# Kernel optimization log

Measured on AMD Instinct MI355X. Metric: run time of the kernel, lower is better.

## Reference

```python
import jax, jax.numpy as jnp
import numpy as np

EPS = 1e-8  # torch cosine_similarity eps


def _first_occurrence_mask(ids, n, k, half):
    # ids: [half] int indices into [0,n). Returns boolean mask of the first k
    # distinct ids in order of first occurrence (torch.unique + slice semantics).
    pos = jnp.arange(half, dtype=jnp.int32)
    occ = jnp.full((n,), half, dtype=jnp.int32).at[ids].min(pos)  # first occurrence position, half if absent
    order = jnp.argsort(occ)
    rank = jnp.zeros((n,), jnp.int32).at[order].set(jnp.arange(n, dtype=jnp.int32))
    return (rank < k) & (occ < half)


def _split_rows(emb, mask, k):
    # emb: [n,h]; selected rows (mask) go to 'mutual' (in index order, zero-padded
    # to k), remaining rows go to 'only' (in index order, zero-padded).
    n = emb.shape[0]
    idx = jnp.arange(n)
    order = jnp.argsort(jnp.where(mask, idx, idx + n))  # selected first, index order
    sel_first = mask[order]
    g = emb[order]
    mutual = g[:k] * sel_first[:k, None].astype(emb.dtype)
    only = g[k:] * (~sel_first[k:])[:, None].astype(emb.dtype)
    return mutual, only


def _split_one(v, t, kv, kt, half):
    # v: [Vl,H], t: [Tl,H]
    Vl, H = v.shape
    Tl = t.shape[0]
    vnorm = jnp.linalg.norm(v, axis=-1)  # [Vl]
    tnorm = jnp.linalg.norm(t, axis=-1)  # [Tl]
    sims = (v @ t.T) / jnp.maximum(vnorm[:, None] * tnorm[None, :], EPS)  # [Vl,Tl]
    top_idx = jnp.argsort(-sims.reshape(-1))[:half]
    vid = (top_idx // Tl).astype(jnp.int32)
    tid = (top_idx % Tl).astype(jnp.int32)
    mask_v = _first_occurrence_mask(vid, Vl, kv, half)
    mask_t = _first_occurrence_mask(tid, Tl, kt, half)
    v_mut, v_only = _split_rows(v, mask_v, kv)
    t_mut, t_only = _split_rows(t, mask_t, kt)
    return v_mut, t_mut, v_only, t_only


def setup_inputs() -> dict:
    key = jax.random.key(0)
    k1, k2 = jax.random.split(key)
    B, Vl, Tl, H = 64, 256, 512, 512
    return {
        "video_embeddings": jax.random.normal(k1, (B, Vl, H), dtype=jnp.float32),
        "text_embeddings": jax.random.normal(k2, (B, Tl, H), dtype=jnp.float32),
    }


def reference(video_embeddings, text_embeddings):
    B, Vl, H = video_embeddings.shape
    Tl = text_embeddings.shape[1]
    half = (Vl * Tl) // 2
    kv = (Vl - 1) // 2  # replicates source loop-variable slice bug
    kt = (Tl - 1) // 2
    fn = lambda v, t: _split_one(v, t, kv, kt, half)
    return jax.vmap(fn)(video_embeddings, text_embeddings)
```

## Files before the change

kernel.cpp:

```cpp
#include <hip/hip_runtime.h>
#include <math.h>

#define B_  64
#define VL 256
#define TL 512
#define HD 512
#define KV 127
#define KT 255
#define EPSF 1e-8f

typedef __attribute__((ext_vector_type(8))) short short8;
typedef __attribute__((ext_vector_type(4))) float f32x4;

#define WS_ROWP  0
#define WS_COLP  (B_*2*VL)
#define WS_SRC   (WS_COLP + B_*2*TL)

__device__ __forceinline__ unsigned fkey(float f) {
    unsigned u = __float_as_uint(f);
    return (u & 0x80000000u) ? ~u : (u | 0x80000000u);
}

__device__ __forceinline__ unsigned cvt_pk_bf16(float a, float b) {
    unsigned r;
    asm("v_cvt_pk_bf16_f32 %0, %1, %2" : "=v"(r) : "v"(a), "v"(b));
    return r;
}

__device__ __forceinline__ void split_pair(float a, float b, unsigned& hh, unsigned& ll, float& ss) {
    ss = fmaf(a, a, ss);
    ss = fmaf(b, b, ss);
    unsigned ua = __float_as_uint(a) & 0xFFFF0000u;
    unsigned ub = __float_as_uint(b) & 0xFFFF0000u;
    hh = __builtin_amdgcn_perm(ub, ua, 0x07060302u);
    ll = cvt_pk_bf16(a - __uint_as_float(ua), b - __uint_as_float(ub));
}

__device__ __forceinline__ void cvt_store8(unsigned* __restrict__ ph, unsigned* __restrict__ pl,
                                           float4 x0, float4 x1, float& ss) {
    unsigned hh0, hh1, hh2, hh3, ll0, ll1, ll2, ll3;
    split_pair(x0.x, x0.y, hh0, ll0, ss);
    split_pair(x0.z, x0.w, hh1, ll1, ss);
    split_pair(x1.x, x1.y, hh2, ll2, ss);
    split_pair(x1.z, x1.w, hh3, ll3, ss);
    *(uint4*)ph = (uint4){hh0, hh1, hh2, hh3};
    *(uint4*)pl = (uint4){ll0, ll1, ll2, ll3};
}

__global__ __launch_bounds__(512, 2) void k_simmax(const float* __restrict__ video,
                                                   const float* __restrict__ text,
                                                   unsigned* __restrict__ rowp,
                                                   unsigned* __restrict__ colp) {
    __shared__ __align__(16) unsigned pA[2][2][2048];
    __shared__ __align__(16) unsigned pB[2][2][4096];
    __shared__ float vns_s[128], tns_s[256];
    __shared__ unsigned rowm[128], colm[256];

    int bb = blockIdx.x;
    int z = bb & 7, w = bb >> 3;
    int b  = z * 8 + (w >> 2);
    int mt = (w >> 1) & 1, nt = w & 1;
    int m0 = mt * 128, n0 = nt * 256;

    const float* Vb = video + (size_t)b * VL * HD;
    const float* Tb = text  + (size_t)b * TL * HD;

    int tid = threadIdx.x;
    int l = tid & 63, wid = tid >> 6;
    int fr = l & 15, g = l >> 4;
    int wm = (wid >> 2) * 64, wn = (wid & 3) * 64;

    int rA = tid >> 2, c = tid & 3;
    int rB0 = rA, rB1 = 128 + rA;
    unsigned wA  = rA  * 16 + (c ^ ((rA  >> 1) & 3)) * 4;
    unsigned wB0 = rB0 * 16 + (c ^ ((rB0 >> 1) & 3)) * 4;
    unsigned wB1 = rB1 * 16 + (c ^ ((rB1 >> 1) & 3)) * 4;
    const float* aptr  = Vb + (size_t)(m0 + rA)  * HD + c * 8;
    const float* bptr0 = Tb + (size_t)(n0 + rB0) * HD + c * 8;
    const float* bptr1 = Tb + (size_t)(n0 + rB1) * HD + c * 8;

    f32x4 acc[4][4];
#pragma unroll
    for (int i = 0; i < 4; ++i)
#pragma unroll
        for (int j = 0; j < 4; ++j) acc[i][j] = (f32x4){0.f, 0.f, 0.f, 0.f};

    float sa = 0.f, sb0 = 0.f, sb1 = 0.f;

    float4 a0  = *(const float4*)(aptr),      a1  = *(const float4*)(aptr + 4);
    float4 b00 = *(const float4*)(bptr0),     b01 = *(const float4*)(bptr0 + 4);
    float4 b10 = *(const float4*)(bptr1),     b11 = *(const float4*)(bptr1 + 4);
    cvt_store8(&pA[0][0][wA],  &pA[0][1][wA],  a0,  a1,  sa);
    cvt_store8(&pB[0][0][wB0], &pB[0][1][wB0], b00, b01, sb0);
    cvt_store8(&pB[0][0][wB1], &pB[0][1][wB1], b10, b11, sb1);
    a0  = *(const float4*)(aptr + 32);  a1  = *(const float4*)(aptr + 36);
    b00 = *(const float4*)(bptr0 + 32); b01 = *(const float4*)(bptr0 + 36);
    b10 = *(const float4*)(bptr1 + 32); b11 = *(const float4*)(bptr1 + 36);
    __syncthreads();

    for (int t = 0; t < 16; ++t) {
        int cur = t & 1, nxt = cur ^ 1;
        short8 fah[4], fal[4], fbh[4], fbl[4];
#pragma unroll
        for (int i = 0; i < 4; ++i) {
            int row = wm + i * 16 + fr;
            unsigned ridx = row * 16 + (g ^ ((row >> 1) & 3)) * 4;
            fah[i] = *(const short8*)&pA[cur][0][ridx];
            fal[i] = *(const short8*)&pA[cur][1][ridx];
        }
#pragma unroll
        for (int j = 0; j < 4; ++j) {
            int row = wn + j * 16 + fr;
            unsigned ridx = row * 16 + (g ^ ((row >> 1) & 3)) * 4;
            fbh[j] = *(const short8*)&pB[cur][0][ridx];
            fbl[j] = *(const short8*)&pB[cur][1][ridx];
        }
        if (t < 15) {
            cvt_store8(&pA[nxt][0][wA],  &pA[nxt][1][wA],  a0,  a1,  sa);
            cvt_store8(&pB[nxt][0][wB0], &pB[nxt][1][wB0], b00, b01, sb0);
            cvt_store8(&pB[nxt][0][wB1], &pB[nxt][1][wB1], b10, b11, sb1);
            if (t < 14) {
                const float* ap  = aptr  + (t + 2) * 32;
                const float* bp0 = bptr0 + (t + 2) * 32;
                const float* bp1 = bptr1 + (t + 2) * 32;
                a0  = *(const float4*)ap;  a1  = *(const float4*)(ap + 4);
                b00 = *(const float4*)bp0; b01 = *(const float4*)(bp0 + 4);
                b10 = *(const float4*)bp1; b11 = *(const float4*)(bp1 + 4);
            }
        }
#pragma unroll
        for (int j = 0; j < 4; ++j)
#pragma unroll
            for (int i = 0; i < 4; ++i)
                acc[i][j] = __builtin_amdgcn_mfma_f32_16x16x32_bf16(fah[i], fbh[j], acc[i][j], 0, 0, 0);
#pragma unroll
        for (int j = 0; j < 4; ++j)
#pragma unroll
            for (int i = 0; i < 4; ++i)
                acc[i][j] = __builtin_amdgcn_mfma_f32_16x16x32_bf16(fal[i], fbh[j], acc[i][j], 0, 0, 0);
#pragma unroll
        for (int j = 0; j < 4; ++j)
#pragma unroll
            for (int i = 0; i < 4; ++i)
                acc[i][j] = __builtin_amdgcn_mfma_f32_16x16x32_bf16(fah[i], fbl[j], acc[i][j], 0, 0, 0);
        __syncthreads();
    }

    sa  += __shfl_xor(sa, 1, 64);  sa  += __shfl_xor(sa, 2, 64);
    sb0 += __shfl_xor(sb0, 1, 64); sb0 += __shfl_xor(sb0, 2, 64);
    sb1 += __shfl_xor(sb1, 1, 64); sb1 += __shfl_xor(sb1, 2, 64);
    if (c == 0) {
        vns_s[rA]  = sqrtf(sa);
        tns_s[rB0] = sqrtf(sb0);
        tns_s[rB1] = sqrtf(sb1);
    }
    if (tid < 128) rowm[tid] = 0u;
    if (tid >= 128 && tid < 384) colm[tid - 128] = 0u;
    __syncthreads();

    float vr[16], tc[4];
#pragma unroll
    for (int i = 0; i < 4; ++i)
#pragma unroll
        for (int r = 0; r < 4; ++r) vr[i * 4 + r] = vns_s[wm + i * 16 + g * 4 + r];
#pragma unroll
    for (int j = 0; j < 4; ++j) tc[j] = tns_s[wn + j * 16 + fr];

    float rmx[16], cmx[4];
#pragma unroll
    for (int i = 0; i < 16; ++i) rmx[i] = -INFINITY;
#pragma unroll
    for (int j = 0; j < 4; ++j) cmx[j] = -INFINITY;
#pragma unroll
    for (int i = 0; i < 4; ++i)
#pragma unroll
        for (int j = 0; j < 4; ++j)
#pragma unroll
            for (int r = 0; r < 4; ++r) {
                float s = acc[i][j][r] / fmaxf(vr[i * 4 + r] * tc[j], EPSF);
                rmx[i * 4 + r] = fmaxf(rmx[i * 4 + r], s);
                cmx[j]         = fmaxf(cmx[j], s);
            }
#pragma unroll
    for (int off = 1; off < 16; off <<= 1)
#pragma unroll
        for (int i = 0; i < 16; ++i) rmx[i] = fmaxf(rmx[i], __shfl_xor(rmx[i], off, 64));
#pragma unroll
    for (int off = 16; off < 64; off <<= 1)
#pragma unroll
        for (int j = 0; j < 4; ++j) cmx[j] = fmaxf(cmx[j], __shfl_xor(cmx[j], off, 64));
    if (fr == 0) {
#pragma unroll
        for (int i = 0; i < 4; ++i)
#pragma unroll
            for (int r = 0; r < 4; ++r)
                atomicMax(&rowm[wm + i * 16 + g * 4 + r], fkey(rmx[i * 4 + r]));
    }
    if (g == 0) {
#pragma unroll
        for (int j = 0; j < 4; ++j) atomicMax(&colm[wn + j * 16 + fr], fkey(cmx[j]));
    }
    __syncthreads();
    if (tid < 128)      rowp[(b * 2 + nt) * VL + m0 + tid] = rowm[tid];
    else if (tid < 384) colp[(b * 2 + mt) * TL + n0 + (tid - 128)] = colm[tid - 128];
}

__global__ __launch_bounds__(512) void k_select(const unsigned* __restrict__ rowp,
                                                const unsigned* __restrict__ colp,
                                                int* __restrict__ srcidx) {
    __shared__ __align__(16) unsigned rk[VL];
    __shared__ __align__(16) unsigned ck[TL];
    __shared__ int wsumv[4], wsumt[8];
    int b = blockIdx.x, tid = threadIdx.x;
    int lane = tid & 63, wv = tid >> 6;
    if (tid < VL) rk[tid] = max(rowp[(b * 2 + 0) * VL + tid], rowp[(b * 2 + 1) * VL + tid]);
    ck[tid] = max(colp[(b * 2 + 0) * TL + tid], colp[(b * 2 + 1) * TL + tid]);
    for (int i = tid; i < 768; i += 512) srcidx[b * 768 + i] = -1;
    __syncthreads();

    int flagv = 0;
    if (tid < VL) {
        unsigned me = rk[tid];
        int cnt = 0;
        for (int jb = 0; jb < VL / 4; ++jb) {
            uint4 k4 = *(const uint4*)&rk[jb * 4];
            cnt += (k4.x > me) + (k4.y > me) + (k4.z > me) + (k4.w > me);
            cnt += (k4.x == me && (jb * 4 + 0) < tid) + (k4.y == me && (jb * 4 + 1) < tid)
                 + (k4.z == me && (jb * 4 + 2) < tid) + (k4.w == me && (jb * 4 + 3) < tid);
        }
        flagv = (cnt < KV) ? 1 : 0;
    }
    int flagt;
    {
        unsigned me = ck[tid];
        int cnt = 0;
        for (int jb = 0; jb < TL / 4; ++jb) {
            uint4 k4 = *(const uint4*)&ck[jb * 4];
            cnt += (k4.x > me) + (k4.y > me) + (k4.z > me) + (k4.w > me);
            cnt += (k4.x == me && (jb * 4 + 0) < tid) + (k4.y == me && (jb * 4 + 1) < tid)
                 + (k4.z == me && (jb * 4 + 2) < tid) + (k4.w == me && (jb * 4 + 3) < tid);
        }
        flagt = (cnt < KT) ? 1 : 0;
    }

    unsigned long long mv = __ballot(flagv);
    unsigned long long mtk = __ballot(flagt);
    if (lane == 0) {
        if (wv < 4) wsumv[wv] = __popcll(mv);
        wsumt[wv] = __popcll(mtk);
    }
    __syncthreads();

    unsigned long long ltmask = (1ull << lane) - 1ull;
    if (tid < VL) {
        int base = 0;
#pragma unroll
        for (int w2 = 0; w2 < 4; ++w2) base += (w2 < wv) ? wsumv[w2] : 0;
        int mV = wsumv[0] + wsumv[1] + wsumv[2] + wsumv[3];
        int ps = base + __popcll(mv & ltmask);
        int pu = tid - ps;
        if (flagv) srcidx[b * 768 + ps] = tid;
        else {
            int pos = pu - (KV - mV);
            if (pos >= 0 && pos < VL - KV) srcidx[b * 768 + 382 + pos] = tid;
        }
    }
    {
        int base = 0;
#pragma unroll
        for (int w2 = 0; w2 < 8; ++w2) base += (w2 < wv) ? wsumt[w2] : 0;
        int mT = 0;
#pragma unroll
        for (int w2 = 0; w2 < 8; ++w2) mT += wsumt[w2];
        int ps = base + __popcll(mtk & ltmask);
        int pu = tid - ps;
        if (flagt) srcidx[b * 768 + 127 + ps] = tid;
        else {
            int pos = pu - (KT - mT);
            if (pos >= 0 && pos < TL - KT) srcidx[b * 768 + 511 + pos] = tid;
        }
    }
}

__global__ __launch_bounds__(256) void k_gather(const float* __restrict__ video,
                                                const float* __restrict__ text,
                                                const int* __restrict__ srcidx,
                                                float* __restrict__ out) {
    int row  = blockIdx.x * 4 + (threadIdx.x >> 6);
    int lane = threadIdx.x & 63;
    int b, base, L;
    const float* tens;
    const int S0 = B_ * KV, S1 = S0 + B_ * KT, S2 = S1 + B_ * (VL - KV);
    if (row < S0)      { b = row / KV;            base = 0   + row % KV;            tens = video; L = VL; }
    else if (row < S1) { int r = row - S0; b = r / KT;       base = 127 + r % KT;       tens = text;  L = TL; }
    else if (row < S2) { int r = row - S1; b = r / (VL - KV); base = 382 + r % (VL - KV); tens = video; L = VL; }
    else               { int r = row - S2; b = r / (TL - KT); base = 511 + r % (TL - KT); tens = text;  L = TL; }
    int s = srcidx[b * 768 + base];
    float* op = out + (size_t)row * HD;
    if (s >= 0) {
        const float* sp = tens + ((size_t)b * L + s) * HD;
#pragma unroll
        for (int it = 0; it < 2; ++it)
            *(float4*)(op + lane * 4 + it * 256) = *(const float4*)(sp + lane * 4 + it * 256);
    } else {
        float4 zv = {0.f, 0.f, 0.f, 0.f};
#pragma unroll
        for (int it = 0; it < 2; ++it)
            *(float4*)(op + lane * 4 + it * 256) = zv;
    }
}

extern "C" void kernel_launch(void* const* d_in, const int* in_sizes, int n_in,
                              void* d_out, int out_size, void* d_ws, size_t ws_size,
                              hipStream_t stream) {
    const float* video = (const float*)d_in[0];
    const float* text  = (const float*)d_in[1];
    float*    ws     = (float*)d_ws;
    unsigned* rowp   = (unsigned*)(ws + WS_ROWP);
    unsigned* colp   = (unsigned*)(ws + WS_COLP);
    int*      srcidx = (int*)(ws + WS_SRC);
    float*    out    = (float*)d_out;

    k_simmax<<<256,             512, 0, stream>>>(video, text, rowp, colp);
    k_select<<<B_,              512, 0, stream>>>(rowp, colp, srcidx);
    k_gather<<<(B_ * 768) / 4,  256, 0, stream>>>(video, text, srcidx, out);
}
```

Before: 86.65 us.

## Split similarity-max GEMM into 128x128 tiles across 512 blocks; nontemporal gather stores

The similarity/max kernel now uses 128x128 output tiles with 256-thread blocks, so it launches 512 blocks instead of 256 with 512 threads. The aim is to fill more CUs on the 256-CU device and cut the tail imbalance. Row partial maxima grow from 2 to 4 per batch, so the select kernel now reduces four partials. The gather kernel switches to nontemporal stores for its output. The trade-off is that text and video rows are loaded and converted more often across blocks, and rowp needs more workspace.

Result: slower. 89.89 us (+3.7%).

```diff
diff --git a/kernel.cpp b/kernel.cpp
--- a/kernel.cpp
+++ b/kernel.cpp
@@ -13,7 +13,7 @@
 typedef __attribute__((ext_vector_type(4))) float f32x4;
 
 #define WS_ROWP  0
-#define WS_COLP  (B_*2*VL)
+#define WS_COLP  (B_*4*VL)
 #define WS_SRC   (WS_COLP + B_*2*TL)
 
 __device__ __forceinline__ unsigned fkey(float f) {
@@ -47,20 +47,20 @@
     *(uint4*)pl = (uint4){ll0, ll1, ll2, ll3};
 }
 
-__global__ __launch_bounds__(512, 2) void k_simmax(const float* __restrict__ video,
+__global__ __launch_bounds__(256, 2) void k_simmax(const float* __restrict__ video,
                                                    const float* __restrict__ text,
                                                    unsigned* __restrict__ rowp,
                                                    unsigned* __restrict__ colp) {
     __shared__ __align__(16) unsigned pA[2][2][2048];
-    __shared__ __align__(16) unsigned pB[2][2][4096];
-    __shared__ float vns_s[128], tns_s[256];
-    __shared__ unsigned rowm[128], colm[256];
+    __shared__ __align__(16) unsigned pB[2][2][2048];
+    __shared__ float vns_s[128], tns_s[128];
+    __shared__ unsigned rowm[128], colm[128];
 
     int bb = blockIdx.x;
-    int z = bb & 7, w = bb >> 3;
-    int b  = z * 8 + (w >> 2);
-    int mt = (w >> 1) & 1, nt = w & 1;
-    int m0 = mt * 128, n0 = nt * 256;
+    int z = bb & 7, y = (bb >> 3) & 7, x = bb >> 6;
+    int b  = z * 8 + x;
+    int mt = y >> 2, nt = y & 3;
+    int m0 = mt * 128, n0 = nt * 128;
 
     const float* Vb = video + (size_t)b * VL * HD;
     const float* Tb = text  + (size_t)b * TL * HD;
@@ -68,16 +68,15 @@
     int tid = threadIdx.x;
     int l = tid & 63, wid = tid >> 6;
     int fr = l & 15, g = l >> 4;
-    int wm = (wid >> 2) * 64, wn = (wid & 3) * 64;
-
-    int rA = tid >> 2, c = tid & 3;
-    int rB0 = rA, rB1 = 128 + rA;
-    unsigned wA  = rA  * 16 + (c ^ ((rA  >> 1) & 3)) * 4;
-    unsigned wB0 = rB0 * 16 + (c ^ ((rB0 >> 1) & 3)) * 4;
-    unsigned wB1 = rB1 * 16 + (c ^ ((rB1 >> 1) & 3)) * 4;
-    const float* aptr  = Vb + (size_t)(m0 + rA)  * HD + c * 8;
-    const float* bptr0 = Tb + (size_t)(n0 + rB0) * HD + c * 8;
-    const float* bptr1 = Tb + (size_t)(n0 + rB1) * HD + c * 8;
+    int wm = (wid >> 1) * 64, wn = (wid & 1) * 64;
+
+    int rS = tid >> 1;
+    int c0 = (tid & 1) * 2;
+    unsigned sw = (rS >> 1) & 3;
+    unsigned w0 = rS * 16 + ((unsigned)c0       ^ sw) * 4;
+    unsigned w1 = rS * 16 + ((unsigned)(c0 + 1) ^ sw) * 4;
+    const float* aptr = Vb + (size_t)(m0 + rS) * HD + c0 * 8;
+    const float* bptr = Tb + (size_t)(n0 + rS) * HD + c0 * 8;
 
     f32x4 acc[4][4];
 #pragma unroll
@@ -85,17 +84,20 @@
 #pragma unroll
         for (int j = 0; j < 4; ++j) acc[i][j] = (f32x4){0.f, 0.f, 0.f, 0.f};
 
-    float sa = 0.f, sb0 = 0.f, sb1 = 0.f;
-
-    float4 a0  = *(const float4*)(aptr),      a1  = *(const float4*)(aptr + 4);
-    float4 b00 = *(const float4*)(bptr0),     b01 = *(const float4*)(bptr0 + 4);
-    float4 b10 = *(const float4*)(bptr1),     b11 = *(const float4*)(bptr1 + 4);
-    cvt_store8(&pA[0][0][wA],  &pA[0][1][wA],  a0,  a1,  sa);
-    cvt_store8(&pB[0][0][wB0], &pB[0][1][wB0], b00, b01, sb0);
-    cvt_store8(&pB[0][0][wB1], &pB[0][1][wB1], b10, b11, sb1);
-    a0  = *(const float4*)(aptr + 32);  a1  = *(const float4*)(aptr + 36);
-    b00 = *(const float4*)(bptr0 + 32); b01 = *(const float4*)(bptr0 + 36);
-    b10 = *(const float4*)(bptr1 + 32); b11 = *(const float4*)(bptr1 + 36);
+    float sa = 0.f, sb = 0.f;
+
+    float4 a0 = *(const float4*)(aptr),      a1 = *(const float4*)(aptr + 4);
+    float4 a2 = *(const float4*)(aptr + 8),  a3 = *(const float4*)(aptr + 12);
+    float4 b0 = *(const float4*)(bptr),      b1 = *(const float4*)(bptr + 4);
+    float4 b2 = *(const float4*)(bptr + 8),  b3 = *(const float4*)(bptr + 12);
+    cvt_store8(&pA[0][0][w0], &pA[0][1][w0], a0, a1, sa);
+    cvt_store8(&pA[0][0][w1], &pA[0][1][w1], a2, a3, sa);
+    cvt_store8(&pB[0][0][w0], &pB[0][1][w0], b0, b1, sb);
+    cvt_store8(&pB[0][0][w1], &pB[0][1][w1], b2, b3, sb);
+    a0 = *(const float4*)(aptr + 32); a1 = *(const float4*)(aptr + 36);
+    a2 = *(const float4*)(aptr + 40); a3 = *(const float4*)(aptr + 44);
+    b0 = *(const float4*)(bptr + 32); b1 = *(const float4*)(bptr + 36);
+    b2 = *(const float4*)(bptr + 40); b3 = *(const float4*)(bptr + 44);
     __syncthreads();
 
     for (int t = 0; t < 16; ++t) {
@@ -116,16 +118,17 @@
             fbl[j] = *(const short8*)&pB[cur][1][ridx];
         }
         if (t < 15) {
-            cvt_store8(&pA[nxt][0][wA],  &pA[nxt][1][wA],  a0,  a1,  sa);
-            cvt_store8(&pB[nxt][0][wB0], &pB[nxt][1][wB0], b00, b01, sb0);
-            cvt_store8(&pB[nxt][0][wB1], &pB[nxt][1][wB1], b10, b11, sb1);
+            cvt_store8(&pA[nxt][0][w0], &pA[nxt][1][w0], a0, a1, sa);
+            cvt_store8(&pA[nxt][0][w1], &pA[nxt][1][w1], a2, a3, sa);
+            cvt_store8(&pB[nxt][0][w0], &pB[nxt][1][w0], b0, b1, sb);
+            cvt_store8(&pB[nxt][0][w1], &pB[nxt][1][w1], b2, b3, sb);
             if (t < 14) {
-                const float* ap  = aptr  + (t + 2) * 32;
-                const float* bp0 = bptr0 + (t + 2) * 32;
-                const float* bp1 = bptr1 + (t + 2) * 32;
-                a0  = *(const float4*)ap;  a1  = *(const float4*)(ap + 4);
-                b00 = *(const float4*)bp0; b01 = *(const float4*)(bp0 + 4);
-                b10 = *(const float4*)bp1; b11 = *(const float4*)(bp1 + 4);
+                const float* ap = aptr + (t + 2) * 32;
+                const float* bp = bptr + (t + 2) * 32;
+                a0 = *(const float4*)ap;        a1 = *(const float4*)(ap + 4);
+                a2 = *(const float4*)(ap + 8);  a3 = *(const float4*)(ap + 12);
+                b0 = *(const float4*)bp;        b1 = *(const float4*)(bp + 4);
+                b2 = *(const float4*)(bp + 8);  b3 = *(const float4*)(bp + 12);
             }
         }
 #pragma unroll
@@ -146,16 +149,11 @@
         __syncthreads();
     }
 
-    sa  += __shfl_xor(sa, 1, 64);  sa  += __shfl_xor(sa, 2, 64);
-    sb0 += __shfl_xor(sb0, 1, 64); sb0 += __shfl_xor(sb0, 2, 64);
-    sb1 += __shfl_xor(sb1, 1, 64); sb1 += __shfl_xor(sb1, 2, 64);
-    if (c == 0) {
-        vns_s[rA]  = sqrtf(sa);
-        tns_s[rB0] = sqrtf(sb0);
-        tns_s[rB1] = sqrtf(sb1);
-    }
+    sa += __shfl_xor(sa, 1, 64);
+    sb += __shfl_xor(sb, 1, 64);
+    if ((tid & 1) == 0) { vns_s[rS] = sqrtf(sa); tns_s[rS] = sqrtf(sb); }
     if (tid < 128) rowm[tid] = 0u;
-    if (tid >= 128 && tid < 384) colm[tid - 128] = 0u;
+    else           colm[tid - 128] = 0u;
     __syncthreads();
 
     float vr[16], tc[4];
@@ -201,8 +199,8 @@
         for (int j = 0; j < 4; ++j) atomicMax(&colm[wn + j * 16 + fr], fkey(cmx[j]));
     }
     __syncthreads();
-    if (tid < 128)      rowp[(b * 2 + nt) * VL + m0 + tid] = rowm[tid];
-    else if (tid < 384) colp[(b * 2 + mt) * TL + n0 + (tid - 128)] = colm[tid - 128];
+    if (tid < 128) rowp[(b * 4 + nt) * VL + m0 + tid] = rowm[tid];
+    else           colp[(b * 2 + mt) * TL + n0 + (tid - 128)] = colm[tid - 128];
 }
 
 __global__ __launch_bounds__(512) void k_select(const unsigned* __restrict__ rowp,
@@ -213,7 +211,11 @@
     __shared__ int wsumv[4], wsumt[8];
     int b = blockIdx.x, tid = threadIdx.x;
     int lane = tid & 63, wv = tid >> 6;
-    if (tid < VL) rk[tid] = max(rowp[(b * 2 + 0) * VL + tid], rowp[(b * 2 + 1) * VL + tid]);
+    if (tid < VL) {
+        unsigned m = max(max(rowp[(b * 4 + 0) * VL + tid], rowp[(b * 4 + 1) * VL + tid]),
+                         max(rowp[(b * 4 + 2) * VL + tid], rowp[(b * 4 + 3) * VL + tid]));
+        rk[tid] = m;
+    }
     ck[tid] = max(colp[(b * 2 + 0) * TL + tid], colp[(b * 2 + 1) * TL + tid]);
     for (int i = tid; i < 768; i += 512) srcidx[b * 768 + i] = -1;
     __syncthreads();
@@ -300,13 +302,15 @@
     if (s >= 0) {
         const float* sp = tens + ((size_t)b * L + s) * HD;
 #pragma unroll
+        for (int it = 0; it < 2; ++it) {
+            f32x4 v = *(const f32x4*)(sp + lane * 4 + it * 256);
+            __builtin_nontemporal_store(v, (f32x4*)(op + lane * 4 + it * 256));
+        }
+    } else {
+        f32x4 zv = {0.f, 0.f, 0.f, 0.f};
+#pragma unroll
         for (int it = 0; it < 2; ++it)
-            *(float4*)(op + lane * 4 + it * 256) = *(const float4*)(sp + lane * 4 + it * 256);
-    } else {
-        float4 zv = {0.f, 0.f, 0.f, 0.f};
-#pragma unroll
-        for (int it = 0; it < 2; ++it)
-            *(float4*)(op + lane * 4 + it * 256) = zv;
+            __builtin_nontemporal_store(zv, (f32x4*)(op + lane * 4 + it * 256));
     }
 }
 
@@ -321,7 +325,7 @@
     int*      srcidx = (int*)(ws + WS_SRC);
     float*    out    = (float*)d_out;
 
-    k_simmax<<<256,             512, 0, stream>>>(video, text, rowp, colp);
+    k_simmax<<<B_ * 8,          256, 0, stream>>>(video, text, rowp, colp);
     k_select<<<B_,              512, 0, stream>>>(rowp, colp, srcidx);
     k_gather<<<(B_ * 768) / 4,  256, 0, stream>>>(video, text, srcidx, out);
 }
```

## Fuse simmax, select and gather into one kernel with per-batch atomic handoff

Applied to the files above, without the earlier changes.

Merges the three kernels into a single launch. The last of the four tiles of each batch to finish, detected with an atomic counter, runs the top-k selection. The other three tiles spin on a per-batch flag, and then all four tiles gather their share of output rows. This removes two kernel launches and their gaps, at the cost of a memset, spin-waiting blocks and launch_bounds occupancy dropping to one block per CU. The spin wait depends on all 256 blocks being co-resident to avoid deadlock.

After: 150.7 us. 73.9% more time.

```diff
diff --git a/kernel.cpp b/kernel.cpp
--- a/kernel.cpp
+++ b/kernel.cpp
@@ -12,8 +12,10 @@
 typedef __attribute__((ext_vector_type(8))) short short8;
 typedef __attribute__((ext_vector_type(4))) float f32x4;
 
-#define WS_ROWP  0
-#define WS_COLP  (B_*2*VL)
+#define WS_CNT   0
+#define WS_FLAG  (B_)
+#define WS_ROWP  (2*B_)
+#define WS_COLP  (WS_ROWP + B_*2*VL)
 #define WS_SRC   (WS_COLP + B_*2*TL)
 
 __device__ __forceinline__ unsigned fkey(float f) {
@@ -47,19 +49,35 @@
     *(uint4*)pl = (uint4){ll0, ll1, ll2, ll3};
 }
 
-__global__ __launch_bounds__(512, 2) void k_simmax(const float* __restrict__ video,
-                                                   const float* __restrict__ text,
-                                                   unsigned* __restrict__ rowp,
-                                                   unsigned* __restrict__ colp) {
+__device__ __forceinline__ void ast(unsigned* p, unsigned v) {
+    __hip_atomic_store(p, v, __ATOMIC_RELAXED, __HIP_MEMORY_SCOPE_AGENT);
+}
+__device__ __forceinline__ unsigned ald(const unsigned* p) {
+    return __hip_atomic_load(p, __ATOMIC_RELAXED, __HIP_MEMORY_SCOPE_AGENT);
+}
+
+__global__ __launch_bounds__(512, 1) void k_fused(const float* __restrict__ video,
+                                                  const float* __restrict__ text,
+                                                  unsigned* __restrict__ cnt,
+                                                  unsigned* __restrict__ flag,
+                                                  unsigned* __restrict__ rowp,
+                                                  unsigned* __restrict__ colp,
+                                                  unsigned* __restrict__ srcidx,
+                                                  float* __restrict__ out) {
     __shared__ __align__(16) unsigned pA[2][2][2048];
     __shared__ __align__(16) unsigned pB[2][2][4096];
     __shared__ float vns_s[128], tns_s[256];
     __shared__ unsigned rowm[128], colm[256];
+    __shared__ __align__(16) unsigned rk[VL];
+    __shared__ __align__(16) unsigned ck[TL];
+    __shared__ int wsumv[4], wsumt[8];
+    __shared__ int sh_last;
 
     int bb = blockIdx.x;
     int z = bb & 7, w = bb >> 3;
     int b  = z * 8 + (w >> 2);
     int mt = (w >> 1) & 1, nt = w & 1;
+    int q  = w & 3;
     int m0 = mt * 128, n0 = nt * 256;
 
     const float* Vb = video + (size_t)b * VL * HD;
@@ -201,112 +219,119 @@
         for (int j = 0; j < 4; ++j) atomicMax(&colm[wn + j * 16 + fr], fkey(cmx[j]));
     }
     __syncthreads();
-    if (tid < 128)      rowp[(b * 2 + nt) * VL + m0 + tid] = rowm[tid];
-    else if (tid < 384) colp[(b * 2 + mt) * TL + n0 + (tid - 128)] = colm[tid - 128];
-}
-
-__global__ __launch_bounds__(512) void k_select(const unsigned* __restrict__ rowp,
-                                                const unsigned* __restrict__ colp,
-                                                int* __restrict__ srcidx) {
-    __shared__ __align__(16) unsigned rk[VL];
-    __shared__ __align__(16) unsigned ck[TL];
-    __shared__ int wsumv[4], wsumt[8];
-    int b = blockIdx.x, tid = threadIdx.x;
-    int lane = tid & 63, wv = tid >> 6;
-    if (tid < VL) rk[tid] = max(rowp[(b * 2 + 0) * VL + tid], rowp[(b * 2 + 1) * VL + tid]);
-    ck[tid] = max(colp[(b * 2 + 0) * TL + tid], colp[(b * 2 + 1) * TL + tid]);
-    for (int i = tid; i < 768; i += 512) srcidx[b * 768 + i] = -1;
-    __syncthreads();
-
-    int flagv = 0;
-    if (tid < VL) {
-        unsigned me = rk[tid];
-        int cnt = 0;
-        for (int jb = 0; jb < VL / 4; ++jb) {
-            uint4 k4 = *(const uint4*)&rk[jb * 4];
-            cnt += (k4.x > me) + (k4.y > me) + (k4.z > me) + (k4.w > me);
-            cnt += (k4.x == me && (jb * 4 + 0) < tid) + (k4.y == me && (jb * 4 + 1) < tid)
-                 + (k4.z == me && (jb * 4 + 2) < tid) + (k4.w == me && (jb * 4 + 3) < tid);
-        }
-        flagv = (cnt < KV) ? 1 : 0;
-    }
-    int flagt;
-    {
-        unsigned me = ck[tid];
-        int cnt = 0;
-        for (int jb = 0; jb < TL / 4; ++jb) {
-            uint4 k4 = *(const uint4*)&ck[jb * 4];
-            cnt += (k4.x > me) + (k4.y > me) + (k4.z > me) + (k4.w > me);
-            cnt += (k4.x == me && (jb * 4 + 0) < tid) + (k4.y == me && (jb * 4 + 1) < tid)
-                 + (k4.z == me && (jb * 4 + 2) < tid) + (k4.w == me && (jb * 4 + 3) < tid);
-        }
-        flagt = (cnt < KT) ? 1 : 0;
-    }
-
-    unsigned long long mv = __ballot(flagv);
-    unsigned long long mtk = __ballot(flagt);
-    if (lane == 0) {
-        if (wv < 4) wsumv[wv] = __popcll(mv);
-        wsumt[wv] = __popcll(mtk);
-    }
-    __syncthreads();
-
-    unsigned long long ltmask = (1ull << lane) - 1ull;
-    if (tid < VL) {
-        int base = 0;
-#pragma unroll
-        for (int w2 = 0; w2 < 4; ++w2) base += (w2 < wv) ? wsumv[w2] : 0;
-        int mV = wsumv[0] + wsumv[1] + wsumv[2] + wsumv[3];
-        int ps = base + __popcll(mv & ltmask);
-        int pu = tid - ps;
-        if (flagv) srcidx[b * 768 + ps] = tid;
-        else {
-            int pos = pu - (KV - mV);
-            if (pos >= 0 && pos < VL - KV) srcidx[b * 768 + 382 + pos] = tid;
-        }
-    }
-    {
-        int base = 0;
-#pragma unroll
-        for (int w2 = 0; w2 < 8; ++w2) base += (w2 < wv) ? wsumt[w2] : 0;
-        int mT = 0;
-#pragma unroll
-        for (int w2 = 0; w2 < 8; ++w2) mT += wsumt[w2];
-        int ps = base + __popcll(mtk & ltmask);
-        int pu = tid - ps;
-        if (flagt) srcidx[b * 768 + 127 + ps] = tid;
-        else {
-            int pos = pu - (KT - mT);
-            if (pos >= 0 && pos < TL - KT) srcidx[b * 768 + 511 + pos] = tid;
-        }
-    }
-}
-
-__global__ __launch_bounds__(256) void k_gather(const float* __restrict__ video,
-                                                const float* __restrict__ text,
-                                                const int* __restrict__ srcidx,
-                                                float* __restrict__ out) {
-    int row  = blockIdx.x * 4 + (threadIdx.x >> 6);
-    int lane = threadIdx.x & 63;
-    int b, base, L;
-    const float* tens;
-    const int S0 = B_ * KV, S1 = S0 + B_ * KT, S2 = S1 + B_ * (VL - KV);
-    if (row < S0)      { b = row / KV;            base = 0   + row % KV;            tens = video; L = VL; }
-    else if (row < S1) { int r = row - S0; b = r / KT;       base = 127 + r % KT;       tens = text;  L = TL; }
-    else if (row < S2) { int r = row - S1; b = r / (VL - KV); base = 382 + r % (VL - KV); tens = video; L = VL; }
-    else               { int r = row - S2; b = r / (TL - KT); base = 511 + r % (TL - KT); tens = text;  L = TL; }
-    int s = srcidx[b * 768 + base];
-    float* op = out + (size_t)row * HD;
-    if (s >= 0) {
-        const float* sp = tens + ((size_t)b * L + s) * HD;
-#pragma unroll
-        for (int it = 0; it < 2; ++it)
-            *(float4*)(op + lane * 4 + it * 256) = *(const float4*)(sp + lane * 4 + it * 256);
+
+    if (tid < 128)      ast(&rowp[(b * 2 + nt) * VL + m0 + tid], rowm[tid]);
+    else if (tid < 384) ast(&colp[(b * 2 + mt) * TL + n0 + (tid - 128)], colm[tid - 128]);
+    __threadfence();
+    __syncthreads();
+    if (tid == 0) {
+        unsigned old = __hip_atomic_fetch_add(&cnt[b], 1u, __ATOMIC_ACQ_REL, __HIP_MEMORY_SCOPE_AGENT);
+        sh_last = (old == 3u);
+    }
+    __syncthreads();
+
+    if (sh_last) {
+        int lane = l, wv = wid;
+        if (tid < VL) rk[tid] = max(ald(&rowp[(b * 2 + 0) * VL + tid]), ald(&rowp[(b * 2 + 1) * VL + tid]));
+        ck[tid] = max(ald(&colp[(b * 2 + 0) * TL + tid]), ald(&colp[(b * 2 + 1) * TL + tid]));
+        for (int i = tid; i < 768; i += 512) ast(&srcidx[b * 768 + i], 0xFFFFFFFFu);
+        __syncthreads();
+
+        int flagv = 0;
+        if (tid < VL) {
+            unsigned me = rk[tid];
+            int cnt2 = 0;
+            for (int jb = 0; jb < VL / 4; ++jb) {
+                uint4 k4 = *(const uint4*)&rk[jb * 4];
+                cnt2 += (k4.x > me) + (k4.y > me) + (k4.z > me) + (k4.w > me);
+                cnt2 += (k4.x == me && (jb * 4 + 0) < tid) + (k4.y == me && (jb * 4 + 1) < tid)
+                      + (k4.z == me && (jb * 4 + 2) < tid) + (k4.w == me && (jb * 4 + 3) < tid);
+            }
+            flagv = (cnt2 < KV) ? 1 : 0;
+        }
+        int flagt;
+        {
+            unsigned me = ck[tid];
+            int cnt2 = 0;
+            for (int jb = 0; jb < TL / 4; ++jb) {
+                uint4 k4 = *(const uint4*)&ck[jb * 4];
+                cnt2 += (k4.x > me) + (k4.y > me) + (k4.z > me) + (k4.w > me);
+                cnt2 += (k4.x == me && (jb * 4 + 0) < tid) + (k4.y == me && (jb * 4 + 1) < tid)
+                      + (k4.z == me && (jb * 4 + 2) < tid) + (k4.w == me && (jb * 4 + 3) < tid);
+            }
+            flagt = (cnt2 < KT) ? 1 : 0;
+        }
+
+        unsigned long long mv = __ballot(flagv);
+        unsigned long long mtk = __ballot(flagt);
+        if (lane == 0) {
+            if (wv < 4) wsumv[wv] = __popcll(mv);
+            wsumt[wv] = __popcll(mtk);
+        }
+        __syncthreads();
+
+        unsigned long long ltmask = (1ull << lane) - 1ull;
+        if (tid < VL) {
+            int base = 0;
+#pragma unroll
+            for (int w2 = 0; w2 < 4; ++w2) base += (w2 < wv) ? wsumv[w2] : 0;
+            int mV = wsumv[0] + wsumv[1] + wsumv[2] + wsumv[3];
+            int ps = base + __popcll(mv & ltmask);
+            int pu = tid - ps;
+            if (flagv) ast(&srcidx[b * 768 + ps], (unsigned)tid);
+            else {
+                int pos = pu - (KV - mV);
+                if (pos >= 0 && pos < VL - KV) ast(&srcidx[b * 768 + 382 + pos], (unsigned)tid);
+            }
+        }
+        {
+            int base = 0;
+#pragma unroll
+            for (int w2 = 0; w2 < 8; ++w2) base += (w2 < wv) ? wsumt[w2] : 0;
+            int mT = 0;
+#pragma unroll
+            for (int w2 = 0; w2 < 8; ++w2) mT += wsumt[w2];
+            int ps = base + __popcll(mtk & ltmask);
+            int pu = tid - ps;
+            if (flagt) ast(&srcidx[b * 768 + 127 + ps], (unsigned)tid);
+            else {
+                int pos = pu - (KT - mT);
+                if (pos >= 0 && pos < TL - KT) ast(&srcidx[b * 768 + 511 + pos], (unsigned)tid);
+            }
+        }
+        __threadfence();
+        __syncthreads();
+        if (tid == 0) __hip_atomic_store(&flag[b], 1u, __ATOMIC_RELEASE, __HIP_MEMORY_SCOPE_AGENT);
     } else {
-        float4 zv = {0.f, 0.f, 0.f, 0.f};
-#pragma unroll
-        for (int it = 0; it < 2; ++it)
-            *(float4*)(op + lane * 4 + it * 256) = zv;
+        if (tid == 0) {
+            while (__hip_atomic_load(&flag[b], __ATOMIC_ACQUIRE, __HIP_MEMORY_SCOPE_AGENT) == 0u)
+                __builtin_amdgcn_s_sleep(8);
+        }
+        __syncthreads();
+    }
+
+    for (int it = 0; it < 24; ++it) {
+        int li = q * 192 + wid * 24 + it;
+        int srow = (int)ald(&srcidx[b * 768 + li]);
+        size_t orow;
+        const float* tens;
+        int L;
+        if (li < 127)      { orow = (size_t)b * KV + li;                              tens = Vb; L = VL; }
+        else if (li < 382) { orow = (size_t)B_ * KV + (size_t)b * KT + (li - 127);    tens = Tb; L = TL; }
+        else if (li < 511) { orow = (size_t)B_ * (KV + KT) + (size_t)b * (VL - KV) + (li - 382); tens = Vb; L = VL; }
+        else               { orow = (size_t)B_ * (KV + KT + VL - KV) + (size_t)b * (TL - KT) + (li - 511); tens = Tb; L = TL; }
+        float* op = out + orow * HD;
+        if (srow >= 0) {
+            const float* sp = tens + (size_t)srow * HD;
+#pragma unroll
+            for (int h = 0; h < 2; ++h)
+                *(float4*)(op + l * 4 + h * 256) = *(const float4*)(sp + l * 4 + h * 256);
+        } else {
+            float4 zv = {0.f, 0.f, 0.f, 0.f};
+#pragma unroll
+            for (int h = 0; h < 2; ++h)
+                *(float4*)(op + l * 4 + h * 256) = zv;
+        }
     }
 }
 
@@ -315,13 +340,14 @@
                               hipStream_t stream) {
     const float* video = (const float*)d_in[0];
     const float* text  = (const float*)d_in[1];
-    float*    ws     = (float*)d_ws;
-    unsigned* rowp   = (unsigned*)(ws + WS_ROWP);
-    unsigned* colp   = (unsigned*)(ws + WS_COLP);
-    int*      srcidx = (int*)(ws + WS_SRC);
+    unsigned* ws     = (unsigned*)d_ws;
+    unsigned* cnt    = ws + WS_CNT;
+    unsigned* flg    = ws + WS_FLAG;
+    unsigned* rowp   = ws + WS_ROWP;
+    unsigned* colp   = ws + WS_COLP;
+    unsigned* srcidx = ws + WS_SRC;
     float*    out    = (float*)d_out;
 
-    k_simmax<<<256,             512, 0, stream>>>(video, text, rowp, colp);
-    k_select<<<B_,              512, 0, stream>>>(rowp, colp, srcidx);
-    k_gather<<<(B_ * 768) / 4,  256, 0, stream>>>(video, text, srcidx, out);
-}
+    hipMemsetAsync(cnt, 0, 2 * B_ * sizeof(unsigned), stream);
+    k_fused<<<256, 512, 0, stream>>>(video, text, cnt, flg, rowp, colp, srcidx, out);
+}
```
